# Kernel optimization log

Measured on AMD Instinct MI355X. Metric: run time of the kernel, lower is better.

The kernel has to match this reference:

```python
import jax, jax.numpy as jnp
import numpy as np

NUM_CAPSULE = 16
DIM_CAPSULE = 64
ROUTINGS = 3
T_EPS = 1e-07


def squash(v, axis=-1):
    # NOTE: this repo's 'squash' is v / sqrt(||v||^2 + eps) (norm-only scaling)
    s = jnp.sum(v * v, axis=axis, keepdims=True)
    return v / jnp.sqrt(s + T_EPS)


def setup_inputs() -> dict:
    key = jax.random.key(0)
    k1, k2 = jax.random.split(key)
    B, N_in, D_in = 64, 512, 1024
    x = jax.random.normal(k1, (B, N_in, D_in), dtype=jnp.float32)
    # xavier-normal-ish init for W [1, D_in, num_capsule*dim_capsule]
    fan_in, fan_out = D_in, NUM_CAPSULE * DIM_CAPSULE
    std = float(np.sqrt(2.0 / (fan_in + fan_out)))
    W = jax.random.normal(k2, (1, D_in, NUM_CAPSULE * DIM_CAPSULE), dtype=jnp.float32) * std
    return {"x": x, "W": W}


def reference(x, W):
    B, N_in, D_in = x.shape
    # u_hat: [B, N_in, num_cap*dim_cap] -> [B, num_cap, N_in, dim_cap]
    u_hat = jnp.matmul(x, W[0])
    u_hat = u_hat.reshape(B, N_in, NUM_CAPSULE, DIM_CAPSULE).transpose(0, 2, 1, 3)
    b = jnp.zeros((B, NUM_CAPSULE, N_in), dtype=u_hat.dtype)
    outputs = None
    for i in range(ROUTINGS):
        # torch code permutes to [B, N_in, num_cap], softmaxes dim=2, permutes back:
        # equivalent to softmax over the num_capsule axis (axis=1)
        c = jax.nn.softmax(b, axis=1)  # [B, num_cap, N_in]
        outputs = squash(jnp.einsum('bij,bijk->bik', c, u_hat))  # [B, num_cap, dim_cap]
        if i < ROUTINGS - 1:
            b = jnp.einsum('bik,bijk->bij', outputs, u_hat)  # [B, num_cap, N_in]
    return outputs
```

## Files before the change

kernel.cpp:

```cpp
#include <hip/hip_runtime.h>
#include <stdint.h>

#define NUM_CAP 16
#define DIM_CAP 64
#define BATCH   64
#define N_IN    512
#define D_IN    1024
#define N_COL   1024
#define M_ROWS  (BATCH*N_IN)

typedef __attribute__((ext_vector_type(8))) short short8;
typedef __attribute__((ext_vector_type(4))) float f32x4;

__device__ __forceinline__ float bf2f(unsigned int u) {
  return __uint_as_float(u << 16);
}
__device__ __forceinline__ unsigned short f2bf_rne(float f) {
  unsigned int x = __float_as_uint(f);
  x += 0x7fffu + ((x >> 16) & 1u);
  return (unsigned short)(x >> 16);
}
__device__ __forceinline__ unsigned int pack_rne(unsigned int lo, unsigned int hi) {
  const unsigned int lr = lo + (0x7fffu + ((lo >> 16) & 1u));
  const unsigned int hr = hi + (0x7fffu + ((hi >> 16) & 1u));
  return (lr >> 16) | (hr & 0xffff0000u);
}

__global__ __launch_bounds__(256) void conv_x(const float* __restrict__ x,
                                              unsigned short* __restrict__ xb) {
  const size_t i = ((size_t)blockIdx.x * 256 + threadIdx.x) * 8;
  const uint4 a = *(const uint4*)(x + i);
  const uint4 b = *(const uint4*)(x + i + 4);
  uint4 p;
  p.x = pack_rne(a.x, a.y); p.y = pack_rne(a.z, a.w);
  p.z = pack_rne(b.x, b.y); p.w = pack_rne(b.z, b.w);
  *(uint4*)(xb + i) = p;
}

__global__ void transpose_w(const float* __restrict__ W,
                            unsigned short* __restrict__ Wt) {
  __shared__ float tile[32][33];
  const int tx = threadIdx.x, ty = threadIdx.y;
  const int bx = blockIdx.x, by = blockIdx.y;
  tile[ty][tx] = W[(by * 32 + ty) * N_COL + bx * 32 + tx];
  __syncthreads();
  Wt[(bx * 32 + ty) * D_IN + by * 32 + tx] = f2bf_rne(tile[tx][ty]);
}

__global__ __launch_bounds__(256) void zero_s1(float* __restrict__ S1) {
  *(float4*)(S1 + ((size_t)blockIdx.x * 256 + threadIdx.x) * 4) =
      make_float4(0.f, 0.f, 0.f, 0.f);
}

__global__ __launch_bounds__(256) void gemm_uhat(
    const unsigned short* __restrict__ A,
    const unsigned short* __restrict__ Bt,
    unsigned short* __restrict__ C,
    float* __restrict__ S1) {
  __shared__ __align__(16) unsigned short lA[128 * 32];
  __shared__ __align__(16) unsigned short lB[128 * 32];
  __shared__ float cs[128];

  const int t = threadIdx.x;
  const int wave = t >> 6, lane = t & 63;
  const int xcd = blockIdx.x & 7, local = blockIdx.x >> 3;
  const int mt = xcd * 32 + (local >> 3), nt = local & 7;
  const int m0 = mt * 128, n0 = nt * 128;
  const int wm = wave & 1, wn = wave >> 1;

  if (t < 128) cs[t] = 0.f;

  f32x4 acc[4][4] = {};

  const int srow = lane >> 2;
  const int schunk = ((lane & 3) ^ ((srow >> 1) & 3)) * 8;

  for (int kt = 0; kt < D_IN / 32; ++kt) {
    const int k0 = kt * 32;
    __syncthreads();
    #pragma unroll
    for (int s0 = 0; s0 < 2; ++s0) {
      const int s = wave + s0 * 4;
      const unsigned short* ga = A + (size_t)(m0 + s * 16 + srow) * D_IN + k0 + schunk;
      __builtin_amdgcn_global_load_lds(
          (const __attribute__((address_space(1))) void*)ga,
          (__attribute__((address_space(3))) void*)(lA + s * 512), 16, 0, 0);
      const unsigned short* gb = Bt + (size_t)(n0 + s * 16 + srow) * D_IN + k0 + schunk;
      __builtin_amdgcn_global_load_lds(
          (const __attribute__((address_space(1))) void*)gb,
          (__attribute__((address_space(3))) void*)(lB + s * 512), 16, 0, 0);
    }
    __syncthreads();

    short8 af[4], bfr[4];
    const int rsel = lane & 15;
    const int q = lane >> 4;
    const int koff = (q ^ ((rsel >> 1) & 3)) * 8;
    #pragma unroll
    for (int tm = 0; tm < 4; tm++)
      af[tm] = *(const short8*)&lA[(wm * 64 + tm * 16 + rsel) * 32 + koff];
    #pragma unroll
    for (int tn = 0; tn < 4; tn++)
      bfr[tn] = *(const short8*)&lB[(wn * 64 + tn * 16 + rsel) * 32 + koff];
    #pragma unroll
    for (int tm = 0; tm < 4; tm++)
      #pragma unroll
      for (int tn = 0; tn < 4; tn++)
        acc[tm][tn] = __builtin_amdgcn_mfma_f32_16x16x32_bf16(
            af[tm], bfr[tn], acc[tm][tn], 0, 0, 0);
  }

  const int lrow = (lane >> 4) * 4, lcol = lane & 15;
  #pragma unroll
  for (int tm = 0; tm < 4; tm++)
    #pragma unroll
    for (int tn = 0; tn < 4; tn++)
      #pragma unroll
      for (int r = 0; r < 4; r++) {
        const int row = m0 + wm * 64 + tm * 16 + lrow + r;
        const int col = n0 + wn * 64 + tn * 16 + lcol;
        C[(size_t)row * N_COL + col] = f2bf_rne(acc[tm][tn][r]);
      }

  #pragma unroll
  for (int tn = 0; tn < 4; tn++) {
    float p = 0.f;
    #pragma unroll
    for (int tm = 0; tm < 4; tm++)
      #pragma unroll
      for (int r = 0; r < 4; r++) p += acc[tm][tn][r];
    atomicAdd(&cs[wn * 64 + tn * 16 + lcol], p);
  }
  __syncthreads();
  if (t < 128)
    atomicAdd(&S1[(size_t)(mt >> 2) * N_COL + n0 + t], cs[t] * 0.0625f);
}

__global__ __launch_bounds__(256) void route_mid(
    const unsigned short* __restrict__ uhat,
    const float* __restrict__ Vin,
    float* __restrict__ Pout,
    const int mode) {
  __shared__ float sq[16 * 68];
  __shared__ float red[4][1024];
  const int t = threadIdx.x;
  const int w = t >> 6, lane = t & 63;
  const int b = blockIdx.x >> 4, jt4 = blockIdx.x & 15;
  const int jt = jt4 * 4 + w;
  const int i_l = lane >> 2, c4 = lane & 3;

  float4 v4;
  if (mode == 0) {
    v4 = *(const float4*)&Vin[(size_t)b * 1024 + t * 4];
  } else {
    v4 = make_float4(0.f, 0.f, 0.f, 0.f);
    #pragma unroll
    for (int s = 0; s < 16; ++s) {
      const float4 ps = *(const float4*)&Vin[((size_t)b * 16 + s) * 1024 + t * 4];
      v4.x += ps.x; v4.y += ps.y; v4.z += ps.z; v4.w += ps.w;
    }
  }
  float ss = v4.x * v4.x + v4.y * v4.y + v4.z * v4.z + v4.w * v4.w;
  #pragma unroll
  for (int d = 1; d < 16; d <<= 1) ss += __shfl_xor(ss, d);
  const float inv = 1.f / sqrtf(ss + 1e-7f);
  const int oi = t >> 4, ok = (t & 15) * 4;
  *(float4*)&sq[oi * 68 + ok] = make_float4(v4.x * inv, v4.y * inv, v4.z * inv, v4.w * inv);
  __syncthreads();

  float pv[16];
  #pragma unroll
  for (int q = 0; q < 4; q++)
    *(float4*)&pv[q * 4] = *(const float4*)&sq[i_l * 68 + c4 * 16 + q * 4];

  float acc[16];
  #pragma unroll
  for (int q = 0; q < 16; q++) acc[q] = 0.f;

  const unsigned short* ub =
      uhat + (size_t)(b * N_IN + jt * 8) * N_COL + lane * 16;

  for (int jj = 0; jj < 8; ++jj, ub += N_COL) {
    const uint4 d0 = *(const uint4*)ub;
    const uint4 d1 = *(const uint4*)(ub + 8);
    float u[16];
    #define UNP(wd, o) { u[(o)] = bf2f((wd) & 0xffffu); u[(o)+1] = __uint_as_float((wd) & 0xffff0000u); }
    UNP(d0.x, 0) UNP(d0.y, 2) UNP(d0.z, 4) UNP(d0.w, 6)
    UNP(d1.x, 8) UNP(d1.y, 10) UNP(d1.z, 12) UNP(d1.w, 14)
    #undef UNP

    float dot = 0.f;
    #pragma unroll
    for (int q = 0; q < 16; q++) dot = fmaf(pv[q], u[q], dot);
    dot += __shfl_xor(dot, 1);
    dot += __shfl_xor(dot, 2);
    const float e = __expf(dot);
    float s = e;
    #pragma unroll
    for (int d = 4; d < 64; d <<= 1) s += __shfl_xor(s, d);
    const float c = e / s;
    #pragma unroll
    for (int q = 0; q < 16; q++) acc[q] = fmaf(c, u[q], acc[q]);
  }

  #pragma unroll
  for (int q = 0; q < 4; q++)
    *(float4*)&red[w][lane * 16 + q * 4] = make_float4(
        acc[q * 4 + 0], acc[q * 4 + 1], acc[q * 4 + 2], acc[q * 4 + 3]);
  __syncthreads();
  float4 s4 = make_float4(0.f, 0.f, 0.f, 0.f);
  #pragma unroll
  for (int ww = 0; ww < 4; ++ww) {
    const float4 r = *(const float4*)&red[ww][t * 4];
    s4.x += r.x; s4.y += r.y; s4.z += r.z; s4.w += r.w;
  }
  *(float4*)&Pout[(size_t)blockIdx.x * 1024 + t * 4] = s4;
}

__global__ __launch_bounds__(64) void route_last(
    const float* __restrict__ P, float* __restrict__ dst) {
  const int bi = blockIdx.x;
  const int k = threadIdx.x;
  const int b = bi >> 4, i = bi & 15;
  const float* p = P + (size_t)b * 16 * 1024 + i * 64 + k;
  float s = 0.f;
  #pragma unroll
  for (int tt = 0; tt < 16; ++tt) s += p[(size_t)tt * 1024];
  float ss = s * s;
  #pragma unroll
  for (int d = 1; d < 64; d <<= 1) ss += __shfl_xor(ss, d);
  dst[bi * 64 + k] = s / sqrtf(ss + 1e-7f);
}

extern "C" void kernel_launch(void* const* d_in, const int* in_sizes, int n_in,
                              void* d_out, int out_size, void* d_ws, size_t ws_size,
                              hipStream_t stream) {
  const float* x = (const float*)d_in[0];
  const float* W = (const float*)d_in[1];
  float* out = (float*)d_out;

  char* ws = (char*)d_ws;
  unsigned short* Wt   = (unsigned short*)ws;
  unsigned short* uhat = (unsigned short*)(ws + (size_t)(2 << 20));
  unsigned short* xb   = (unsigned short*)(ws + (size_t)66 * (1 << 20));
  float* S1 = (float*)(ws + (size_t)130 * (1 << 20));
  float* P1 = (float*)(ws + (size_t)66 * (1 << 20));
  float* P2 = (float*)(ws + (size_t)71 * (1 << 20));

  transpose_w<<<dim3(32, 32), dim3(32, 32), 0, stream>>>(W, Wt);
  conv_x<<<16384, 256, 0, stream>>>(x, xb);
  zero_s1<<<64, 256, 0, stream>>>(S1);
  gemm_uhat<<<2048, 256, 0, stream>>>(xb, Wt, uhat, S1);

  route_mid<<<1024, 256, 0, stream>>>(uhat, S1, P1, 0);
  route_mid<<<1024, 256, 0, stream>>>(uhat, P1, P2, 1);
  route_last<<<1024, 64, 0, stream>>>(P2, out);
}
```

Before: 339.2 us.

## Merge prep kernels and move first-iteration column sums out of GEMM epilogue

Combines the x conversion and W transpose into one prep launch and drops the zeroing kernel. The first routing pass's per-batch column sums of u_hat are no longer accumulated with shared and global atomics in the GEMM epilogue. A separate s1q kernel instead re-reads the bf16 u_hat and writes per-strip partial sums, which route_mid then adds up over a configurable strip count. This removes atomics and extra syncs from the GEMM and two launches, at the cost of an extra 64 MB read of u_hat.

```diff
diff --git a/kernel.cpp b/kernel.cpp
--- a/kernel.cpp
+++ b/kernel.cpp
@@ -26,40 +26,43 @@
   return (lr >> 16) | (hr & 0xffff0000u);
 }
 
-__global__ __launch_bounds__(256) void conv_x(const float* __restrict__ x,
-                                              unsigned short* __restrict__ xb) {
-  const size_t i = ((size_t)blockIdx.x * 256 + threadIdx.x) * 8;
-  const uint4 a = *(const uint4*)(x + i);
-  const uint4 b = *(const uint4*)(x + i + 4);
-  uint4 p;
-  p.x = pack_rne(a.x, a.y); p.y = pack_rne(a.z, a.w);
-  p.z = pack_rne(b.x, b.y); p.w = pack_rne(b.z, b.w);
-  *(uint4*)(xb + i) = p;
-}
-
-__global__ void transpose_w(const float* __restrict__ W,
-                            unsigned short* __restrict__ Wt) {
-  __shared__ float tile[32][33];
-  const int tx = threadIdx.x, ty = threadIdx.y;
-  const int bx = blockIdx.x, by = blockIdx.y;
-  tile[ty][tx] = W[(by * 32 + ty) * N_COL + bx * 32 + tx];
-  __syncthreads();
-  Wt[(bx * 32 + ty) * D_IN + by * 32 + tx] = f2bf_rne(tile[tx][ty]);
-}
-
-__global__ __launch_bounds__(256) void zero_s1(float* __restrict__ S1) {
-  *(float4*)(S1 + ((size_t)blockIdx.x * 256 + threadIdx.x) * 4) =
-      make_float4(0.f, 0.f, 0.f, 0.f);
+__global__ __launch_bounds__(256) void prep(
+    const float* __restrict__ x, const float* __restrict__ W,
+    unsigned short* __restrict__ xb, unsigned short* __restrict__ Wt) {
+  const int t = threadIdx.x;
+  if (blockIdx.x < 16384) {
+    const size_t i = ((size_t)blockIdx.x * 256 + t) * 8;
+    const uint4 a = *(const uint4*)(x + i);
+    const uint4 b = *(const uint4*)(x + i + 4);
+    uint4 p;
+    p.x = pack_rne(a.x, a.y); p.y = pack_rne(a.z, a.w);
+    p.z = pack_rne(b.x, b.y); p.w = pack_rne(b.z, b.w);
+    *(uint4*)(xb + i) = p;
+  } else {
+    __shared__ float tile[32][33];
+    const int bid = blockIdx.x - 16384;
+    const int bx = bid & 31, by = bid >> 5;
+    const int tx = t & 31, ty0 = t >> 5;
+    #pragma unroll
+    for (int r = 0; r < 4; r++) {
+      const int ty = ty0 + r * 8;
+      tile[ty][tx] = W[(size_t)(by * 32 + ty) * N_COL + bx * 32 + tx];
+    }
+    __syncthreads();
+    #pragma unroll
+    for (int r = 0; r < 4; r++) {
+      const int ty = ty0 + r * 8;
+      Wt[(size_t)(bx * 32 + ty) * D_IN + by * 32 + tx] = f2bf_rne(tile[tx][ty]);
+    }
+  }
 }
 
 __global__ __launch_bounds__(256) void gemm_uhat(
     const unsigned short* __restrict__ A,
     const unsigned short* __restrict__ Bt,
-    unsigned short* __restrict__ C,
-    float* __restrict__ S1) {
+    unsigned short* __restrict__ C) {
   __shared__ __align__(16) unsigned short lA[128 * 32];
   __shared__ __align__(16) unsigned short lB[128 * 32];
-  __shared__ float cs[128];
 
   const int t = threadIdx.x;
   const int wave = t >> 6, lane = t & 63;
@@ -67,8 +70,6 @@
   const int mt = xcd * 32 + (local >> 3), nt = local & 7;
   const int m0 = mt * 128, n0 = nt * 128;
   const int wm = wave & 1, wn = wave >> 1;
-
-  if (t < 128) cs[t] = 0.f;
 
   f32x4 acc[4][4] = {};
 
@@ -121,26 +122,31 @@
         const int col = n0 + wn * 64 + tn * 16 + lcol;
         C[(size_t)row * N_COL + col] = f2bf_rne(acc[tm][tn][r]);
       }
-
-  #pragma unroll
-  for (int tn = 0; tn < 4; tn++) {
-    float p = 0.f;
-    #pragma unroll
-    for (int tm = 0; tm < 4; tm++)
-      #pragma unroll
-      for (int r = 0; r < 4; r++) p += acc[tm][tn][r];
-    atomicAdd(&cs[wn * 64 + tn * 16 + lcol], p);
-  }
-  __syncthreads();
-  if (t < 128)
-    atomicAdd(&S1[(size_t)(mt >> 2) * N_COL + n0 + t], cs[t] * 0.0625f);
+}
+
+__global__ __launch_bounds__(256) void s1q(
+    const unsigned short* __restrict__ uhat, float* __restrict__ S1q) {
+  const int t = threadIdx.x;
+  const int b = blockIdx.x >> 3, s = blockIdx.x & 7;
+  const unsigned short* up =
+      uhat + (size_t)(b * N_IN + s * 64) * N_COL + t * 4;
+  float4 a = make_float4(0.f, 0.f, 0.f, 0.f);
+  #pragma unroll 8
+  for (int j = 0; j < 64; ++j, up += N_COL) {
+    const uint2 d = *(const uint2*)up;
+    a.x += bf2f(d.x & 0xffffu);
+    a.y += __uint_as_float(d.x & 0xffff0000u);
+    a.z += bf2f(d.y & 0xffffu);
+    a.w += __uint_as_float(d.y & 0xffff0000u);
+  }
+  *(float4*)&S1q[(size_t)blockIdx.x * 1024 + t * 4] = a;
 }
 
 __global__ __launch_bounds__(256) void route_mid(
     const unsigned short* __restrict__ uhat,
     const float* __restrict__ Vin,
     float* __restrict__ Pout,
-    const int mode) {
+    const int nstrips) {
   __shared__ float sq[16 * 68];
   __shared__ float red[4][1024];
   const int t = threadIdx.x;
@@ -149,23 +155,18 @@
   const int jt = jt4 * 4 + w;
   const int i_l = lane >> 2, c4 = lane & 3;
 
-  float4 v4;
-  if (mode == 0) {
-    v4 = *(const float4*)&Vin[(size_t)b * 1024 + t * 4];
-  } else {
-    v4 = make_float4(0.f, 0.f, 0.f, 0.f);
-    #pragma unroll
-    for (int s = 0; s < 16; ++s) {
-      const float4 ps = *(const float4*)&Vin[((size_t)b * 16 + s) * 1024 + t * 4];
-      v4.x += ps.x; v4.y += ps.y; v4.z += ps.z; v4.w += ps.w;
-    }
+  float4 v4 = make_float4(0.f, 0.f, 0.f, 0.f);
+  for (int s = 0; s < nstrips; ++s) {
+    const float4 ps = *(const float4*)&Vin[((size_t)b * nstrips + s) * 1024 + t * 4];
+    v4.x += ps.x; v4.y += ps.y; v4.z += ps.z; v4.w += ps.w;
   }
   float ss = v4.x * v4.x + v4.y * v4.y + v4.z * v4.z + v4.w * v4.w;
   #pragma unroll
   for (int d = 1; d < 16; d <<= 1) ss += __shfl_xor(ss, d);
   const float inv = 1.f / sqrtf(ss + 1e-7f);
   const int oi = t >> 4, ok = (t & 15) * 4;
-  *(float4*)&sq[oi * 68 + ok] = make_float4(v4.x * inv, v4.y * inv, v4.z * inv, v4.w * inv);
+  *(float4*)&sq[oi * 68 + ok] =
+      make_float4(v4.x * inv, v4.y * inv, v4.z * inv, v4.w * inv);
   __syncthreads();
 
   float pv[16];
@@ -247,12 +248,10 @@
   float* P1 = (float*)(ws + (size_t)66 * (1 << 20));
   float* P2 = (float*)(ws + (size_t)71 * (1 << 20));
 
-  transpose_w<<<dim3(32, 32), dim3(32, 32), 0, stream>>>(W, Wt);
-  conv_x<<<16384, 256, 0, stream>>>(x, xb);
-  zero_s1<<<64, 256, 0, stream>>>(S1);
-  gemm_uhat<<<2048, 256, 0, stream>>>(xb, Wt, uhat, S1);
-
-  route_mid<<<1024, 256, 0, stream>>>(uhat, S1, P1, 0);
-  route_mid<<<1024, 256, 0, stream>>>(uhat, P1, P2, 1);
+  prep<<<16384 + 1024, 256, 0, stream>>>(x, W, xb, Wt);
+  gemm_uhat<<<2048, 256, 0, stream>>>(xb, Wt, uhat);
+  s1q<<<512, 256, 0, stream>>>(uhat, S1);
+  route_mid<<<1024, 256, 0, stream>>>(uhat, S1, P1, 8);
+  route_mid<<<1024, 256, 0, stream>>>(uhat, P1, P2, 16);
   route_last<<<1024, 64, 0, stream>>>(P2, out);
 }
```

After: 322.5 us. 1.05x faster.
